# Performance work log

Hardware: AMD Instinct MI355X
Metric: run time of the kernel (lower is better)

## Reference

```python
import jax, jax.numpy as jnp
import numpy as np

B, C, L = 256, 500, 200
D, H, NUM_ITEMS = 64, 128, 100000
BETA = 0.7
EPS = 1e-8


def _xavier(key, fan_in, fan_out):
    lim = float(np.sqrt(6.0 / (fan_in + fan_out)))
    return jax.random.uniform(key, (fan_in, fan_out), minval=-lim, maxval=lim, dtype=jnp.float32)


def setup_inputs() -> dict:
    key = jax.random.key(0)
    ks = jax.random.split(key, 12)
    inp = {
        'candidate_items': jax.random.randint(ks[0], (B, C), 0, NUM_ITEMS, dtype=jnp.int64) if jax.config.read('jax_enable_x64') else jax.random.randint(ks[0], (B, C), 0, NUM_ITEMS),
        'query_times': jax.random.uniform(ks[1], (B,), dtype=jnp.float32),
        'candidate_histories': jax.random.uniform(ks[2], (B, C, L), dtype=jnp.float32),
        'item_emb': 0.02 * jax.random.normal(ks[3], (NUM_ITEMS, D), dtype=jnp.float32),
        'base_W1': _xavier(ks[4], D, H), 'base_b1': jnp.zeros((H,), jnp.float32),
        'base_W2': _xavier(ks[5], H, H), 'base_b2': jnp.zeros((H,), jnp.float32),
        'base_W3': _xavier(ks[6], H, 1),
        'exc_W1': _xavier(ks[7], D, H), 'exc_b1': jnp.zeros((H,), jnp.float32),
        'exc_W2': _xavier(ks[8], H, H), 'exc_b2': jnp.zeros((H,), jnp.float32),
        'exc_W3': _xavier(ks[9], H, 1),
    }
    return inp


def _mlp(x, W1, b1, W2, b2, W3):
    # (Linear + Softplus) x depth, then Linear -> 1 (no bias), squeeze last dim
    h = jax.nn.softplus(x @ W1 + b1)
    h = jax.nn.softplus(h @ W2 + b2)
    return (h @ W3)[..., 0]


def reference(candidate_items, query_times, candidate_histories, item_emb,
              base_W1, base_b1, base_W2, base_b2, base_W3,
              exc_W1, exc_b1, exc_W2, exc_b2, exc_W3):
    z = item_emb[candidate_items]                                  # [B, C, D]
    mu = jax.nn.softplus(_mlp(z, base_W1, base_b1, base_W2, base_b2, base_W3)) + EPS   # [B, C]
    alpha = jax.nn.softplus(_mlp(z, exc_W1, exc_b1, exc_W2, exc_b2, exc_W3)) + EPS     # [B, C]
    q = query_times[:, None, None]                                 # [B, 1, 1]
    mask = candidate_histories < q                                 # [B, C, L]
    delta = jnp.maximum(q - candidate_histories, 0.0)              # clamp(min=0)
    h = jnp.sum(jnp.exp(-BETA * delta) * mask, axis=-1)            # [B, C]
    return mu + alpha * h
```

## Files before the change

kernel.cpp:

```cpp
#include <hip/hip_runtime.h>
#include <math.h>

#define BB 256
#define CC 500
#define LL 200
#define DD 64
#define HH 128
#define NUM_ITEMS 100000
#define BETA 0.7f
#define EPSV 1e-8f

#define TM 32
#define NTILE (NUM_ITEMS / TM)
#define BPS 1024
#define NROW (BB * CC)
#define NBH 8000

typedef _Float16 half8 __attribute__((ext_vector_type(8)));
typedef _Float16 half4 __attribute__((ext_vector_type(4)));
typedef __fp16   pk2   __attribute__((ext_vector_type(2)));
typedef float floatx4 __attribute__((ext_vector_type(4)));

__device__ __forceinline__ float softplus_safe(float x) {
    float t = __expf(-fabsf(x));
    return fmaxf(x, 0.0f) + __logf(1.0f + t);
}
__device__ __forceinline__ float softplus_fast(float x) {
    return __logf(1.0f + __expf(x));
}
__device__ __forceinline__ float softplus_small(float x) {
    float z = x * x;
    float p = fmaf(fmaf(-5.2083333e-3f, z, 0.125f), z, 0.69314718f);
    return fmaf(x, 0.5f, p);
}

__global__ __launch_bounds__(256, 4) void mlp_mfma(
    const float* __restrict__ emb,
    const float* __restrict__ W1, const float* __restrict__ b1,
    const float* __restrict__ W2, const float* __restrict__ b2,
    const float* __restrict__ W3,
    const float* __restrict__ V1, const float* __restrict__ c1,
    const float* __restrict__ V2, const float* __restrict__ c2,
    const float* __restrict__ V3,
    float* __restrict__ ma2)
{
    __shared__ __align__(16) _Float16 h1s[TM * HH];
    __shared__ __align__(16) float    part[TM * 4];
    int tid  = threadIdx.x;
    int w    = tid >> 6, lane = tid & 63;
    int quad = lane >> 4, l15 = lane & 15;

    int is_exc = blockIdx.x >= BPS;
    int bslot  = blockIdx.x - (is_exc ? BPS : 0);

    const float* W1s = is_exc ? V1 : W1;
    const float* W2s = is_exc ? V2 : W2;
    const float* B1s = is_exc ? c1 : b1;
    const float* B2s = is_exc ? c2 : b2;
    const float* W3s = is_exc ? V3 : W3;

    half8 w1f[2][2];
    half8 w2f[4][2];
    floatx4 b1v[2], b2v[2], w3v[2];
    #pragma unroll
    for (int n = 0; n < 2; ++n) {
        int j  = (2 * w + n) * 16 + l15;
        int cb = (2 * w + n) * 16 + quad * 4;
        #pragma unroll
        for (int r = 0; r < 4; ++r) {
            b1v[n][r] = B1s[cb + r];
            b2v[n][r] = B2s[cb + r];
            w3v[n][r] = W3s[cb + r];
        }
        #pragma unroll
        for (int kt = 0; kt < 2; ++kt) {
            half8 h;
            #pragma unroll
            for (int r = 0; r < 8; ++r)
                h[r] = (_Float16)W1s[(kt * 32 + quad * 8 + r) * HH + j];
            w1f[kt][n] = h;
        }
        #pragma unroll
        for (int kt = 0; kt < 4; ++kt) {
            half8 h;
            #pragma unroll
            for (int r = 0; r < 8; ++r)
                h[r] = (_Float16)W2s[(kt * 32 + quad * 8 + r) * HH + j];
            w2f[kt][n] = h;
        }
    }

    const int wc0  = (2 * w) * 2 + (quad >> 1);
    const int wc1  = (2 * w + 1) * 2 + (quad >> 1);
    const int wsub = (quad & 1) * 4;

    #pragma unroll 1
    for (int t = bslot; t < NTILE; t += BPS) {
        half8 zf[2][2];
        #pragma unroll
        for (int mt = 0; mt < 2; ++mt) {
            const float* p = emb + (size_t)(t * TM + mt * 16 + l15) * DD + quad * 8;
            #pragma unroll
            for (int kt = 0; kt < 2; ++kt) {
                floatx4 v0 = *(const floatx4*)(p + kt * 32);
                floatx4 v1 = *(const floatx4*)(p + kt * 32 + 4);
                union { half8 h; pk2 p2[4]; } u;
                u.p2[0] = __builtin_amdgcn_cvt_pkrtz(v0[0], v0[1]);
                u.p2[1] = __builtin_amdgcn_cvt_pkrtz(v0[2], v0[3]);
                u.p2[2] = __builtin_amdgcn_cvt_pkrtz(v1[0], v1[1]);
                u.p2[3] = __builtin_amdgcn_cvt_pkrtz(v1[2], v1[3]);
                zf[mt][kt] = u.h;
            }
        }

        floatx4 acc1[2][2];
        #pragma unroll
        for (int n = 0; n < 2; ++n)
            #pragma unroll
            for (int mt = 0; mt < 2; ++mt) acc1[mt][n] = b1v[n];
        #pragma unroll
        for (int kt = 0; kt < 2; ++kt)
            #pragma unroll
            for (int n = 0; n < 2; ++n)
                #pragma unroll
                for (int mt = 0; mt < 2; ++mt)
                    acc1[mt][n] = __builtin_amdgcn_mfma_f32_16x16x32_f16(
                        w1f[kt][n], zf[mt][kt], acc1[mt][n], 0, 0, 0);
        #pragma unroll
        for (int mt = 0; mt < 2; ++mt)
            #pragma unroll
            for (int n = 0; n < 2; ++n) {
                union { half4 h; pk2 p2[2]; } hu;
                hu.p2[0] = __builtin_amdgcn_cvt_pkrtz(
                    softplus_small(acc1[mt][n][0]), softplus_small(acc1[mt][n][1]));
                hu.p2[1] = __builtin_amdgcn_cvt_pkrtz(
                    softplus_small(acc1[mt][n][2]), softplus_small(acc1[mt][n][3]));
                int wc = n ? wc1 : wc0;
                *(half4*)(&h1s[(mt * 16 + l15) * HH + ((wc ^ l15) * 8) + wsub]) = hu.h;
            }
        __syncthreads();

        floatx4 acc2[2][2];
        #pragma unroll
        for (int n = 0; n < 2; ++n)
            #pragma unroll
            for (int mt = 0; mt < 2; ++mt) acc2[mt][n] = b2v[n];
        #pragma unroll
        for (int kt = 0; kt < 4; ++kt) {
            half8 af[2];
            #pragma unroll
            for (int mt = 0; mt < 2; ++mt)
                af[mt] = *(const half8*)(&h1s[(mt * 16 + l15) * HH +
                                              (((kt * 4 + quad) ^ l15) * 8)]);
            #pragma unroll
            for (int n = 0; n < 2; ++n)
                #pragma unroll
                for (int mt = 0; mt < 2; ++mt)
                    acc2[mt][n] = __builtin_amdgcn_mfma_f32_16x16x32_f16(
                        w2f[kt][n], af[mt], acc2[mt][n], 0, 0, 0);
        }
        #pragma unroll
        for (int mt = 0; mt < 2; ++mt) {
            float sv = 0.0f;
            #pragma unroll
            for (int n = 0; n < 2; ++n)
                #pragma unroll
                for (int r = 0; r < 4; ++r)
                    sv = fmaf(softplus_fast(acc2[mt][n][r]), w3v[n][r], sv);
            sv += __shfl_xor(sv, 16, 64);
            sv += __shfl_xor(sv, 32, 64);
            if (quad == 0)
                part[(mt * 16 + l15) * 4 + w] = sv;
        }
        __syncthreads();

        if (tid < TM) {
            floatx4 pv = *(const floatx4*)(part + tid * 4);
            float s = (pv[0] + pv[1]) + (pv[2] + pv[3]);
            ma2[2 * (t * TM + tid) + is_exc] = softplus_safe(s) + EPSV;
        }
    }
}

__global__ __launch_bounds__(256) void hawkes_kernel(
    const int* __restrict__ items,
    const float* __restrict__ qt,
    const float* __restrict__ hist,
    const float* __restrict__ ma2,
    float* __restrict__ out)
{
    int wv   = blockIdx.x * 4 + (threadIdx.x >> 6);
    int lane = threadIdx.x & 63;
    int r0   = wv * 4;

    bool act = lane < LL / 4;
    int    it[4];
    float  q[4];
    floatx4 v[4];
    #pragma unroll
    for (int i = 0; i < 4; ++i) it[i] = items[r0 + i];
    #pragma unroll
    for (int i = 0; i < 4; ++i) q[i] = qt[(r0 + i) / CC];
    #pragma unroll
    for (int i = 0; i < 4; ++i)
        v[i] = act ? *((const floatx4*)(hist + (size_t)(r0 + i) * LL) + lane)
                   : (floatx4){0.f, 0.f, 0.f, 0.f};
    float2 g[4];
    #pragma unroll
    for (int i = 0; i < 4; ++i) g[i] = *(const float2*)(ma2 + 2 * it[i]);

    #pragma unroll
    for (int i = 0; i < 4; ++i) {
        float s = 0.0f;
        if (act) {
            s  = (v[i][0] < q[i]) ? __expf(BETA * v[i][0]) : 0.f;
            s += (v[i][1] < q[i]) ? __expf(BETA * v[i][1]) : 0.f;
            s += (v[i][2] < q[i]) ? __expf(BETA * v[i][2]) : 0.f;
            s += (v[i][3] < q[i]) ? __expf(BETA * v[i][3]) : 0.f;
        }
        #pragma unroll
        for (int off = 1; off < 64; off <<= 1) s += __shfl_xor(s, off, 64);
        if (lane == 0)
            out[r0 + i] = fmaf(g[i].y * __expf(-BETA * q[i]), s, g[i].x);
    }
}

extern "C" void kernel_launch(void* const* d_in, const int* in_sizes, int n_in,
                              void* d_out, int out_size, void* d_ws, size_t ws_size,
                              hipStream_t stream)
{
    const int*   items = (const int*)  d_in[0];
    const float* qt    = (const float*)d_in[1];
    const float* hist  = (const float*)d_in[2];
    const float* emb   = (const float*)d_in[3];
    const float* W1    = (const float*)d_in[4];
    const float* b1    = (const float*)d_in[5];
    const float* W2    = (const float*)d_in[6];
    const float* b2    = (const float*)d_in[7];
    const float* W3    = (const float*)d_in[8];
    const float* V1    = (const float*)d_in[9];
    const float* c1    = (const float*)d_in[10];
    const float* V2    = (const float*)d_in[11];
    const float* c2    = (const float*)d_in[12];
    const float* V3    = (const float*)d_in[13];

    float* out = (float*)d_out;
    float* ma2 = (float*)d_ws;

    mlp_mfma<<<2 * BPS, 256, 0, stream>>>(emb, W1, b1, W2, b2, W3,
                                          V1, c1, V2, c2, V3, ma2);

    hawkes_kernel<<<NBH, 256, 0, stream>>>(items, qt, hist, ma2, out);
}
```

Before: 232.0 us.

## Prefetch next embedding tile into LDS staging buffer during layer-2 compute

Stages the 32x64 embedding tile through a swizzled fp16 LDS buffer. The global loads for the next tile are issued before the layer-2 MFMAs and converted and written to LDS after them, so load latency overlaps compute. Each thread now loads one contiguous 32-byte chunk, which coalesces better than the old per-lane MFMA-fragment pattern. The cost is extra LDS, more live registers, and a staging write plus read each iteration, which may lower occupancy.

```diff
diff --git a/kernel.cpp b/kernel.cpp
--- a/kernel.cpp
+++ b/kernel.cpp
@@ -45,6 +45,7 @@
     float* __restrict__ ma2)
 {
     __shared__ __align__(16) _Float16 h1s[TM * HH];
+    __shared__ __align__(16) _Float16 z_stage[TM * DD];
     __shared__ __align__(16) float    part[TM * 4];
     int tid  = threadIdx.x;
     int w    = tid >> 6, lane = tid & 63;
@@ -59,6 +60,9 @@
     const float* B2s = is_exc ? c2 : b2;
     const float* W3s = is_exc ? V3 : W3;
 
+    const int sitem = tid >> 3, schunk = tid & 7;
+    const int soff  = sitem * DD + ((schunk ^ (sitem & 7)) * 8);
+
     half8 w1f[2][2];
     half8 w2f[4][2];
     floatx4 b1v[2], b2v[2], w3v[2];
@@ -94,24 +98,30 @@
     const int wc1  = (2 * w + 1) * 2 + (quad >> 1);
     const int wsub = (quad & 1) * 4;
 
+    {
+        const float* ps = emb + (size_t)(bslot * TM + sitem) * DD + schunk * 8;
+        floatx4 s0 = *(const floatx4*)ps;
+        floatx4 s1 = *(const floatx4*)(ps + 4);
+        union { half8 h; pk2 p2[4]; } u;
+        u.p2[0] = __builtin_amdgcn_cvt_pkrtz(s0[0], s0[1]);
+        u.p2[1] = __builtin_amdgcn_cvt_pkrtz(s0[2], s0[3]);
+        u.p2[2] = __builtin_amdgcn_cvt_pkrtz(s1[0], s1[1]);
+        u.p2[3] = __builtin_amdgcn_cvt_pkrtz(s1[2], s1[3]);
+        *(half8*)(&z_stage[soff]) = u.h;
+    }
+    __syncthreads();
+
     #pragma unroll 1
     for (int t = bslot; t < NTILE; t += BPS) {
+        bool more = (t + BPS) < NTILE;
+
         half8 zf[2][2];
         #pragma unroll
-        for (int mt = 0; mt < 2; ++mt) {
-            const float* p = emb + (size_t)(t * TM + mt * 16 + l15) * DD + quad * 8;
-            #pragma unroll
-            for (int kt = 0; kt < 2; ++kt) {
-                floatx4 v0 = *(const floatx4*)(p + kt * 32);
-                floatx4 v1 = *(const floatx4*)(p + kt * 32 + 4);
-                union { half8 h; pk2 p2[4]; } u;
-                u.p2[0] = __builtin_amdgcn_cvt_pkrtz(v0[0], v0[1]);
-                u.p2[1] = __builtin_amdgcn_cvt_pkrtz(v0[2], v0[3]);
-                u.p2[2] = __builtin_amdgcn_cvt_pkrtz(v1[0], v1[1]);
-                u.p2[3] = __builtin_amdgcn_cvt_pkrtz(v1[2], v1[3]);
-                zf[mt][kt] = u.h;
-            }
-        }
+        for (int mt = 0; mt < 2; ++mt)
+            #pragma unroll
+            for (int kt = 0; kt < 2; ++kt)
+                zf[mt][kt] = *(const half8*)(&z_stage[(mt * 16 + l15) * DD +
+                                             (((kt * 4 + quad) ^ (l15 & 7)) * 8)]);
 
         floatx4 acc1[2][2];
         #pragma unroll
@@ -140,6 +150,15 @@
             }
         __syncthreads();
 
+        floatx4 s0 = {0.f, 0.f, 0.f, 0.f}, s1 = {0.f, 0.f, 0.f, 0.f};
+        {
+            const float* ps = emb + (size_t)((t + BPS) * TM + sitem) * DD + schunk * 8;
+            if (more) {
+                s0 = *(const floatx4*)ps;
+                s1 = *(const floatx4*)(ps + 4);
+            }
+        }
+
         floatx4 acc2[2][2];
         #pragma unroll
         for (int n = 0; n < 2; ++n)
@@ -171,6 +190,15 @@
             sv += __shfl_xor(sv, 32, 64);
             if (quad == 0)
                 part[(mt * 16 + l15) * 4 + w] = sv;
+        }
+
+        if (more) {
+            union { half8 h; pk2 p2[4]; } u;
+            u.p2[0] = __builtin_amdgcn_cvt_pkrtz(s0[0], s0[1]);
+            u.p2[1] = __builtin_amdgcn_cvt_pkrtz(s0[2], s0[3]);
+            u.p2[2] = __builtin_amdgcn_cvt_pkrtz(s1[0], s1[1]);
+            u.p2[3] = __builtin_amdgcn_cvt_pkrtz(s1[2], s1[3]);
+            *(half8*)(&z_stage[soff]) = u.h;
         }
         __syncthreads();
 
```

New measurement: 223.9 us. 3.5% less time.
